# Optimization experiments

Hardware: AMD Instinct MI355X
Metric: run time of the kernel (lower is better)

Reference implementation:

```python
import jax, jax.numpy as jnp
import numpy as np

B = 1024
D = 512
M = 65536          # num_memory
C = 4096           # num pseudo-label clusters (= labels.max()+1, fixed for jit)
TEMP = 0.05
EPS = 1e-6


def setup_inputs() -> dict:
    key = jax.random.key(0)
    k1, k2, k3, k4 = jax.random.split(key, 4)
    inputs = jax.random.normal(k1, (B, D), dtype=jnp.float32)
    indexes = jax.random.randint(k2, (B,), 0, M, dtype=jnp.int64)
    feats = jax.random.normal(k3, (M, D), dtype=jnp.float32)
    # memory bank stores L2-normalized features (see _update_feature)
    features = feats / jnp.linalg.norm(feats, axis=1, keepdims=True)
    labels = jax.random.randint(k4, (M,), 0, C, dtype=jnp.int64)
    return {"inputs": inputs, "indexes": indexes, "features": features, "labels": labels}


def reference(inputs, indexes, features, labels):
    # F.normalize(inputs, p=2, dim=1)
    x = inputs / jnp.linalg.norm(inputs, axis=1, keepdims=True)
    # HM.forward: inputs @ features.T, then / temp  -> sim over memory slots [B, M]
    sim = (x @ features.T) / TEMP
    # index_add over labels: per-cluster sum of sim columns  -> [C, B]
    sim_c = jax.ops.segment_sum(sim.T, labels, num_segments=C)
    nums = jax.ops.segment_sum(jnp.ones((M,), dtype=sim.dtype), labels, num_segments=C)  # [C]
    cluster_mask = (nums > 0).astype(sim.dtype)                     # [C]
    # mean within cluster; empty clusters divide by 1
    avg = sim_c / jnp.where(nums > 0, nums, 1.0)[:, None]           # [C, B]
    # masked_softmax over clusters, per sample
    vec = avg.T                                                     # [B, C]
    masked_exps = jnp.exp(vec) * cluster_mask[None, :]
    probs = masked_exps / (jnp.sum(masked_exps, axis=1, keepdims=True) + EPS)
    # F.nll_loss(log(probs + eps), targets) with targets = labels[indexes]
    targets = labels[indexes]                                       # [B]
    logp = jnp.log(probs + EPS)
    loss = -jnp.mean(logp[jnp.arange(B), targets])
    return loss
```

## Files before the change

### kernel.cpp

```cpp
#include <hip/hip_runtime.h>
#include <hip/hip_bf16.h>

#define NB 1024
#define ND 512
#define NM 65536
#define NC 4096

static constexpr float TEMP = 0.05f;
static constexpr float EPSF = 1e-6f;

typedef __attribute__((ext_vector_type(8))) short short8v;
typedef __attribute__((ext_vector_type(16))) float f32x16;

static __device__ __forceinline__ short f2bf(float f) {
    __hip_bfloat16 h = __float2bfloat16(f);
    return *reinterpret_cast<short*>(&h);
}

__global__ __launch_bounds__(128) void k_normalize(const float* __restrict__ in,
                                                   short* __restrict__ xnb) {
    int b = blockIdx.x;
    const float4* row = reinterpret_cast<const float4*>(in + (size_t)b * ND);
    float4 v = row[threadIdx.x];
    float ss = v.x * v.x + v.y * v.y + v.z * v.z + v.w * v.w;
#pragma unroll
    for (int o = 32; o > 0; o >>= 1) ss += __shfl_down(ss, o);
    __shared__ float sw[2];
    int lane = threadIdx.x & 63, w = threadIdx.x >> 6;
    if (lane == 0) sw[w] = ss;
    __syncthreads();
    float inv = 1.0f / sqrtf(sw[0] + sw[1]);
    short4 o;
    o.x = f2bf(v.x * inv); o.y = f2bf(v.y * inv);
    o.z = f2bf(v.z * inv); o.w = f2bf(v.w * inv);
    reinterpret_cast<short4*>(xnb + (size_t)b * ND)[threadIdx.x] = o;
}

__global__ __launch_bounds__(256) void k_count(const int* __restrict__ labels,
                                               int* __restrict__ counts) {
    int m = blockIdx.x * 256 + threadIdx.x;
    if (m < NM) atomicAdd(&counts[labels[m]], 1);
}

__global__ __launch_bounds__(256) void k_scan(const int* __restrict__ counts,
                                              int* __restrict__ starts,
                                              int* __restrict__ cursor) {
    __shared__ int part[256];
    int t = threadIdx.x;
    int local[16];
    int base = t * 16;
    int s = 0;
#pragma unroll
    for (int i = 0; i < 16; ++i) { local[i] = counts[base + i]; s += local[i]; }
    part[t] = s;
    __syncthreads();
    for (int off = 1; off < 256; off <<= 1) {
        int v = (t >= off) ? part[t - off] : 0;
        __syncthreads();
        part[t] += v;
        __syncthreads();
    }
    int excl = (t == 0) ? 0 : part[t - 1];
#pragma unroll
    for (int i = 0; i < 16; ++i) {
        starts[base + i] = excl;
        cursor[base + i] = excl;
        excl += local[i];
    }
}

__global__ __launch_bounds__(256) void k_scatter(const int* __restrict__ labels,
                                                 int* __restrict__ cursor,
                                                 int* __restrict__ idx) {
    int m = blockIdx.x * 256 + threadIdx.x;
    int c = labels[m];
    int pos = atomicAdd(&cursor[c], 1);
    idx[pos] = m;
}

__global__ __launch_bounds__(128) void k_gather(const float* __restrict__ feats,
                                                const int* __restrict__ idx,
                                                const int* __restrict__ starts,
                                                const int* __restrict__ counts,
                                                short* __restrict__ Gb) {
    int c = blockIdx.x;
    int t = threadIdx.x;
    int s0 = starts[c];
    int n = counts[c];
    const float4* F = reinterpret_cast<const float4*>(feats);
    float4 acc = {0.f, 0.f, 0.f, 0.f};
    int m_next = (n > 0) ? idx[s0] : 0;
    for (int j = 0; j < n; ++j) {
        int m = m_next;
        if (j + 1 < n) m_next = idx[s0 + j + 1];
        float4 v = F[(size_t)m * 128 + t];
        acc.x += v.x; acc.y += v.y; acc.z += v.z; acc.w += v.w;
    }
    short4 o;
    o.x = f2bf(acc.x); o.y = f2bf(acc.y); o.z = f2bf(acc.z); o.w = f2bf(acc.w);
    reinterpret_cast<short4*>(Gb + (size_t)c * ND)[t] = o;
}

__global__ __launch_bounds__(256) void k_gemm_mfma(const short* __restrict__ A,
                                                   const short* __restrict__ Bm,
                                                   const int* __restrict__ counts,
                                                   float* __restrict__ out) {
    const int tid = threadIdx.x;
    const int w = tid >> 6;
    const int lane = tid & 63;
    const int ln = lane & 31;
    const int kg = lane >> 5;
    const int row0 = blockIdx.y * 128 + (w >> 1) * 64;
    const int col0 = blockIdx.x * 128 + (w & 1) * 64;

    f32x16 acc00 = {}, acc01 = {}, acc10 = {}, acc11 = {};
    const short* pa0 = A + (size_t)(row0 + ln) * ND + kg * 8;
    const short* pa1 = pa0 + 32 * ND;
    const short* pb0 = Bm + (size_t)(col0 + ln) * ND + kg * 8;
    const short* pb1 = pb0 + 32 * ND;
#pragma unroll 4
    for (int k0 = 0; k0 < ND; k0 += 16) {
        short8v a0 = *reinterpret_cast<const short8v*>(pa0 + k0);
        short8v a1 = *reinterpret_cast<const short8v*>(pa1 + k0);
        short8v b0 = *reinterpret_cast<const short8v*>(pb0 + k0);
        short8v b1 = *reinterpret_cast<const short8v*>(pb1 + k0);
        acc00 = __builtin_amdgcn_mfma_f32_32x32x16_bf16(a0, b0, acc00, 0, 0, 0);
        acc01 = __builtin_amdgcn_mfma_f32_32x32x16_bf16(a0, b1, acc01, 0, 0, 0);
        acc10 = __builtin_amdgcn_mfma_f32_32x32x16_bf16(a1, b0, acc10, 0, 0, 0);
        acc11 = __builtin_amdgcn_mfma_f32_32x32x16_bf16(a1, b1, acc11, 0, 0, 0);
    }
    int colA = col0 + ln;
    int colB = col0 + 32 + ln;
    int nA = counts[colA], nB = counts[colB];
    float invA = 1.0f / (TEMP * (float)(nA > 0 ? nA : 1));
    float invB = 1.0f / (TEMP * (float)(nB > 0 ? nB : 1));
    int rbase = row0 + 4 * kg;
#pragma unroll
    for (int r = 0; r < 16; ++r) {
        int row = rbase + (r & 3) + 8 * (r >> 2);
        out[(size_t)row * NC + colA] = acc00[r] * invA;
        out[(size_t)row * NC + colB] = acc01[r] * invB;
        out[(size_t)(row + 32) * NC + colA] = acc10[r] * invA;
        out[(size_t)(row + 32) * NC + colB] = acc11[r] * invB;
    }
}

__global__ __launch_bounds__(256) void k_loss(const float* __restrict__ avg,
                                              const int* __restrict__ counts,
                                              const int* __restrict__ indexes,
                                              const int* __restrict__ labels,
                                              float* __restrict__ loss_b) {
    int b = blockIdx.x;
    const float* row = avg + (size_t)b * NC;
    float s = 0.f;
    for (int c = threadIdx.x; c < NC; c += 256) {
        if (counts[c] > 0) s += expf(row[c]);
    }
#pragma unroll
    for (int o = 32; o > 0; o >>= 1) s += __shfl_down(s, o);
    __shared__ float sw[4];
    int lane = threadIdx.x & 63, w = threadIdx.x >> 6;
    if (lane == 0) sw[w] = s;
    __syncthreads();
    if (threadIdx.x == 0) {
        float tot = sw[0] + sw[1] + sw[2] + sw[3];
        int t = labels[indexes[b]];
        float p = expf(row[t]) / (tot + EPSF);
        loss_b[b] = -logf(p + EPSF);
    }
}

__global__ __launch_bounds__(256) void k_final(const float* __restrict__ loss_b,
                                               float* __restrict__ out) {
    float s = 0.f;
    for (int i = threadIdx.x; i < NB; i += 256) s += loss_b[i];
#pragma unroll
    for (int o = 32; o > 0; o >>= 1) s += __shfl_down(s, o);
    __shared__ float sw[4];
    int lane = threadIdx.x & 63, w = threadIdx.x >> 6;
    if (lane == 0) sw[w] = s;
    __syncthreads();
    if (threadIdx.x == 0) out[0] = (sw[0] + sw[1] + sw[2] + sw[3]) / (float)NB;
}

extern "C" void kernel_launch(void* const* d_in, const int* in_sizes, int n_in,
                              void* d_out, int out_size, void* d_ws, size_t ws_size,
                              hipStream_t stream) {
    const float* inputs   = (const float*)d_in[0];
    const int*   indexes  = (const int*)d_in[1];
    const float* features = (const float*)d_in[2];
    const int*   labels   = (const int*)d_in[3];
    float* out = (float*)d_out;

    float* avg    = (float*)d_ws;
    short* Gb     = (short*)(avg + (size_t)NB * NC);
    short* xnb    = Gb + (size_t)NC * ND;
    float* loss_b = (float*)(xnb + (size_t)NB * ND);
    int*   counts = (int*)(loss_b + NB);
    int*   starts = counts + NC;
    int*   cursor = starts + NC;
    int*   idx    = cursor + NC;

    hipMemsetAsync(counts, 0, sizeof(int) * NC, stream);

    k_normalize<<<NB, 128, 0, stream>>>(inputs, xnb);
    k_count<<<NM / 256, 256, 0, stream>>>(labels, counts);
    k_scan<<<1, 256, 0, stream>>>(counts, starts, cursor);
    k_scatter<<<NM / 256, 256, 0, stream>>>(labels, cursor, idx);
    k_gather<<<NC, 128, 0, stream>>>(features, idx, starts, counts, Gb);
    dim3 g(NC / 128, NB / 128);
    k_gemm_mfma<<<g, 256, 0, stream>>>(xnb, Gb, counts, avg);
    k_loss<<<NB, 256, 0, stream>>>(avg, counts, indexes, labels, loss_b);
    k_final<<<1, 256, 0, stream>>>(loss_b, out);
}
```

Baseline: 88.21 us.

## Fuse softmax denominator and target gather into GEMM epilogue, drop avg matrix

```diff
diff --git a/kernel.cpp b/kernel.cpp
--- a/kernel.cpp
+++ b/kernel.cpp
@@ -15,6 +15,19 @@
 static __device__ __forceinline__ short f2bf(float f) {
     __hip_bfloat16 h = __float2bfloat16(f);
     return *reinterpret_cast<short*>(&h);
+}
+
+__global__ __launch_bounds__(256) void k_zero_tgt(const int* __restrict__ indexes,
+                                                  const int* __restrict__ labels,
+                                                  int* __restrict__ counts,
+                                                  float* __restrict__ denom,
+                                                  int* __restrict__ tgt) {
+    int i = blockIdx.x * 256 + threadIdx.x;
+    if (i < NC) counts[i] = 0;
+    if (i < NB) {
+        denom[i] = 0.f;
+        tgt[i] = labels[indexes[i]];
+    }
 }
 
 __global__ __launch_bounds__(128) void k_normalize(const float* __restrict__ in,
@@ -88,23 +101,34 @@
     int s0 = starts[c];
     int n = counts[c];
     const float4* F = reinterpret_cast<const float4*>(feats);
-    float4 acc = {0.f, 0.f, 0.f, 0.f};
-    int m_next = (n > 0) ? idx[s0] : 0;
-    for (int j = 0; j < n; ++j) {
-        int m = m_next;
-        if (j + 1 < n) m_next = idx[s0 + j + 1];
-        float4 v = F[(size_t)m * 128 + t];
-        acc.x += v.x; acc.y += v.y; acc.z += v.z; acc.w += v.w;
+    float4 a0 = {0.f, 0.f, 0.f, 0.f};
+    float4 a1 = {0.f, 0.f, 0.f, 0.f};
+    int j = 0;
+    for (; j + 1 < n; j += 2) {
+        int m0 = idx[s0 + j];
+        int m1 = idx[s0 + j + 1];
+        float4 v0 = F[(size_t)m0 * 128 + t];
+        float4 v1 = F[(size_t)m1 * 128 + t];
+        a0.x += v0.x; a0.y += v0.y; a0.z += v0.z; a0.w += v0.w;
+        a1.x += v1.x; a1.y += v1.y; a1.z += v1.z; a1.w += v1.w;
+    }
+    if (j < n) {
+        int m0 = idx[s0 + j];
+        float4 v0 = F[(size_t)m0 * 128 + t];
+        a0.x += v0.x; a0.y += v0.y; a0.z += v0.z; a0.w += v0.w;
     }
     short4 o;
-    o.x = f2bf(acc.x); o.y = f2bf(acc.y); o.z = f2bf(acc.z); o.w = f2bf(acc.w);
+    o.x = f2bf(a0.x + a1.x); o.y = f2bf(a0.y + a1.y);
+    o.z = f2bf(a0.z + a1.z); o.w = f2bf(a0.w + a1.w);
     reinterpret_cast<short4*>(Gb + (size_t)c * ND)[t] = o;
 }
 
 __global__ __launch_bounds__(256) void k_gemm_mfma(const short* __restrict__ A,
                                                    const short* __restrict__ Bm,
                                                    const int* __restrict__ counts,
-                                                   float* __restrict__ out) {
+                                                   const int* __restrict__ tgt,
+                                                   float* __restrict__ denom,
+                                                   float* __restrict__ numer) {
     const int tid = threadIdx.x;
     const int w = tid >> 6;
     const int lane = tid & 63;
@@ -130,50 +154,46 @@
         acc11 = __builtin_amdgcn_mfma_f32_32x32x16_bf16(a1, b1, acc11, 0, 0, 0);
     }
     int colA = col0 + ln;
-    int colB = col0 + 32 + ln;
+    int colB = colA + 32;
     int nA = counts[colA], nB = counts[colB];
     float invA = 1.0f / (TEMP * (float)(nA > 0 ? nA : 1));
     float invB = 1.0f / (TEMP * (float)(nB > 0 ? nB : 1));
+    float mA = (nA > 0) ? 1.f : 0.f;
+    float mB = (nB > 0) ? 1.f : 0.f;
     int rbase = row0 + 4 * kg;
 #pragma unroll
     for (int r = 0; r < 16; ++r) {
         int row = rbase + (r & 3) + 8 * (r >> 2);
-        out[(size_t)row * NC + colA] = acc00[r] * invA;
-        out[(size_t)row * NC + colB] = acc01[r] * invB;
-        out[(size_t)(row + 32) * NC + colA] = acc10[r] * invA;
-        out[(size_t)(row + 32) * NC + colB] = acc11[r] * invB;
-    }
-}
-
-__global__ __launch_bounds__(256) void k_loss(const float* __restrict__ avg,
-                                              const int* __restrict__ counts,
-                                              const int* __restrict__ indexes,
-                                              const int* __restrict__ labels,
-                                              float* __restrict__ loss_b) {
-    int b = blockIdx.x;
-    const float* row = avg + (size_t)b * NC;
-    float s = 0.f;
-    for (int c = threadIdx.x; c < NC; c += 256) {
-        if (counts[c] > 0) s += expf(row[c]);
-    }
-#pragma unroll
-    for (int o = 32; o > 0; o >>= 1) s += __shfl_down(s, o);
-    __shared__ float sw[4];
-    int lane = threadIdx.x & 63, w = threadIdx.x >> 6;
-    if (lane == 0) sw[w] = s;
-    __syncthreads();
-    if (threadIdx.x == 0) {
-        float tot = sw[0] + sw[1] + sw[2] + sw[3];
-        int t = labels[indexes[b]];
-        float p = expf(row[t]) / (tot + EPSF);
-        loss_b[b] = -logf(p + EPSF);
-    }
-}
-
-__global__ __launch_bounds__(256) void k_final(const float* __restrict__ loss_b,
+        int rowH = row + 32;
+        float v00 = acc00[r] * invA, v01 = acc01[r] * invB;
+        float v10 = acc10[r] * invA, v11 = acc11[r] * invB;
+        int t0 = tgt[row], t1 = tgt[rowH];
+        if (t0 == colA) numer[row] = v00;
+        if (t0 == colB) numer[row] = v01;
+        if (t1 == colA) numer[rowH] = v10;
+        if (t1 == colB) numer[rowH] = v11;
+        float s0 = mA * __expf(v00) + mB * __expf(v01);
+        float s1 = mA * __expf(v10) + mB * __expf(v11);
+#pragma unroll
+        for (int m = 1; m < 32; m <<= 1) {
+            s0 += __shfl_xor(s0, m);
+            s1 += __shfl_xor(s1, m);
+        }
+        if (ln == 0) {
+            atomicAdd(&denom[row], s0);
+            atomicAdd(&denom[rowH], s1);
+        }
+    }
+}
+
+__global__ __launch_bounds__(256) void k_final(const float* __restrict__ numer,
+                                               const float* __restrict__ denom,
                                                float* __restrict__ out) {
     float s = 0.f;
-    for (int i = threadIdx.x; i < NB; i += 256) s += loss_b[i];
+    for (int i = threadIdx.x; i < NB; i += 256) {
+        float p = __expf(numer[i]) / (denom[i] + EPSF);
+        s += -logf(p + EPSF);
+    }
 #pragma unroll
     for (int o = 32; o > 0; o >>= 1) s += __shfl_down(s, o);
     __shared__ float sw[4];
@@ -192,24 +212,23 @@
     const int*   labels   = (const int*)d_in[3];
     float* out = (float*)d_out;
 
-    float* avg    = (float*)d_ws;
-    short* Gb     = (short*)(avg + (size_t)NB * NC);
+    short* Gb     = (short*)d_ws;
     short* xnb    = Gb + (size_t)NC * ND;
-    float* loss_b = (float*)(xnb + (size_t)NB * ND);
-    int*   counts = (int*)(loss_b + NB);
+    float* denom  = (float*)(xnb + (size_t)NB * ND);
+    float* numer  = denom + NB;
+    int*   tgt    = (int*)(numer + NB);
+    int*   counts = tgt + NB;
     int*   starts = counts + NC;
     int*   cursor = starts + NC;
     int*   idx    = cursor + NC;
 
-    hipMemsetAsync(counts, 0, sizeof(int) * NC, stream);
-
+    k_zero_tgt<<<16, 256, 0, stream>>>(indexes, labels, counts, denom, tgt);
     k_normalize<<<NB, 128, 0, stream>>>(inputs, xnb);
     k_count<<<NM / 256, 256, 0, stream>>>(labels, counts);
     k_scan<<<1, 256, 0, stream>>>(counts, starts, cursor);
     k_scatter<<<NM / 256, 256, 0, stream>>>(labels, cursor, idx);
     k_gather<<<NC, 128, 0, stream>>>(features, idx, starts, counts, Gb);
     dim3 g(NC / 128, NB / 128);
-    k_gemm_mfma<<<g, 256, 0, stream>>>(xnb, Gb, counts, avg);
-    k_loss<<<NB, 256, 0, stream>>>(avg, counts, indexes, labels, loss_b);
-    k_final<<<1, 256, 0, stream>>>(loss_b, out);
-}
+    k_gemm_mfma<<<g, 256, 0, stream>>>(xnb, Gb, counts, tgt, denom, numer);
+    k_final<<<1, 256, 0, stream>>>(numer, denom, out);
+}
```

Measured after the change: 86.49 us. About the same (-1.9%).
